# Kernel optimization log

Measured on AMD Instinct MI355X. Metric: run time of the kernel, lower is better.

## Reference

```python
import jax, jax.numpy as jnp
import numpy as np

N_NODES = 200000
N_BONDS = 220000
D = 128


def setup_inputs() -> dict:
    key = jax.random.key(0)
    ks = jax.random.split(key, 8)
    h = jax.random.normal(ks[0], (N_NODES, D), dtype=jnp.float32)
    src = jax.random.randint(ks[1], (N_BONDS,), 0, N_NODES, dtype=jnp.int64)
    dst = jax.random.randint(ks[2], (N_BONDS,), 0, N_NODES, dtype=jnp.int64)
    # MLP params (Sequential: Linear(256,128)+ReLU, Linear(128,128)+ReLU, Linear(128,2))
    W1 = jax.random.normal(ks[3], (2 * D, 128), dtype=jnp.float32) * (1.0 / np.sqrt(2 * D))
    b1 = jnp.zeros((128,), dtype=jnp.float32)
    W2 = jax.random.normal(ks[4], (128, 128), dtype=jnp.float32) * (1.0 / np.sqrt(128))
    b2 = jnp.zeros((128,), dtype=jnp.float32)
    W3 = jax.random.normal(ks[5], (128, 2), dtype=jnp.float32) * (1.0 / np.sqrt(128))
    b3 = jnp.zeros((2,), dtype=jnp.float32)
    return {"h": h, "src": src, "dst": dst,
            "W1": W1, "b1": b1, "W2": W2, "b2": b2, "W3": W3, "b3": b3}


def _mlp(x, W1, b1, W2, b2, W3, b3):
    x = jax.nn.relu(x @ W1 + b1)
    x = jax.nn.relu(x @ W2 + b2)
    return x @ W3 + b3


def reference(h, src, dst, W1, b1, W2, b2, W3, b3):
    # forward edges: (src -> dst); reverse edges: (dst -> src)
    h_src = h[src]            # [E, D] gather
    h_dst = h[dst]            # [E, D] gather
    h_forward = jnp.concatenate([h_src, h_dst], axis=1)  # [E, 2D]
    h_reverse = jnp.concatenate([h_dst, h_src], axis=1)  # [E, 2D]
    return (_mlp(h_forward, W1, b1, W2, b2, W3, b3)
            + _mlp(h_reverse, W1, b1, W2, b2, W3, b3))
```

## Files before the change

### kernel.cpp

```cpp
#include <hip/hip_runtime.h>
#include <hip/hip_bf16.h>
#include <stdint.h>


typedef __attribute__((ext_vector_type(8))) short bf16x8;
typedef __attribute__((ext_vector_type(4))) float f32x4;

__device__ __forceinline__ float bf2f(unsigned u16) {
    union { unsigned u; float f; } v; v.u = u16 << 16;
    return v.f;
}
__device__ __forceinline__ unsigned short f2bf(float f) {
    union { float f; unsigned u; } v; v.f = f;
    unsigned u = v.u;
    unsigned r = u + 0x7FFFu + ((u >> 16) & 1u);
    return (unsigned short)(r >> 16);
}

__device__ __forceinline__ int swz(int f, int c) {
    return f * 128 + ((c ^ (f & 7)) << 3);
}

__device__ __forceinline__ bf16x8 cvt8(const float* p) {
    float4 x = *(const float4*)p;
    float4 y = *(const float4*)(p + 4);
    union { bf16x8 v; __hip_bfloat162 h[4]; } R;
    R.h[0] = __float22bfloat162_rn(float2{x.x, x.y});
    R.h[1] = __float22bfloat162_rn(float2{x.z, x.w});
    R.h[2] = __float22bfloat162_rn(float2{y.x, y.y});
    R.h[3] = __float22bfloat162_rn(float2{y.z, y.w});
    return R.v;
}

__device__ __forceinline__ bf16x8 addrelu8(uint4 a, uint4 b) {
    union { uint4 v; unsigned u[4]; } A, B;
    A.v = a; B.v = b;
    union { bf16x8 v; __hip_bfloat162 h[4]; } R;
#pragma unroll
    for (int i = 0; i < 4; ++i) {
        float a0 = bf2f(A.u[i] & 0xFFFFu), a1 = bf2f(A.u[i] >> 16);
        float b0 = bf2f(B.u[i] & 0xFFFFu), b1 = bf2f(B.u[i] >> 16);
        R.h[i] = __float22bfloat162_rn(float2{fmaxf(a0 + b0, 0.f),
                                              fmaxf(a1 + b1, 0.f)});
    }
    return R.v;
}

#define MFMA(a, b, c) __builtin_amdgcn_mfma_f32_16x16x32_bf16((a), (b), (c), 0, 0, 0)

__global__ void prep_weights(const float* __restrict__ W1,
                             const float* __restrict__ W2,
                             unsigned short* __restrict__ W1t,
                             unsigned short* __restrict__ W2t) {
    int idx = blockIdx.x * 256 + threadIdx.x;
    if (idx < 256 * 128) {
        int j = idx >> 7, k = idx & 127;
        float v = (j < 128) ? W1[k * 128 + j] : W1[(k + 128) * 128 + (j - 128)];
        W1t[idx] = f2bf(v);
    } else {
        int i2 = idx - 256 * 128;
        if (i2 < 128 * 128) {
            int n = i2 >> 7, k = i2 & 127;
            W2t[i2] = f2bf(W2[k * 128 + n]);
        }
    }
}

__global__ __launch_bounds__(512, 2) void node_proj(
    const float* __restrict__ h, const unsigned short* __restrict__ W1t,
    const float* __restrict__ b1, unsigned short* __restrict__ P, int nodes) {
    __shared__ unsigned short W1s[256 * 128];

    int t = threadIdx.x;
    int lane = t & 63;
    int wv = t >> 6;
    int ml = lane & 15, quad = lane >> 4;

    {
        int r = t >> 1, half = t & 1;
        const uint4* src = (const uint4*)(W1t + (size_t)r * 128 + half * 64);
#pragma unroll
        for (int i = 0; i < 8; ++i)
            *(uint4*)(W1s + swz(r, half * 8 + i)) = src[i];
    }

    int node = blockIdx.x * 128 + wv * 16 + ml;
    int nodeL = (node < nodes) ? node : (nodes - 1);
    const float* hrow = h + (size_t)nodeL * 128;
    bf16x8 bfrag[4];
#pragma unroll
    for (int kk = 0; kk < 4; ++kk)
        bfrag[kk] = cvt8(hrow + kk * 32 + quad * 8);

    __syncthreads();

    f32x4 acc[16] = {};
#pragma unroll
    for (int kk = 0; kk < 4; ++kk) {
#pragma unroll
        for (int ct = 0; ct < 16; ++ct) {
            bf16x8 afrag = *(const bf16x8*)(W1s + swz(ct * 16 + ml, kk * 4 + quad));
            acc[ct] = MFMA(afrag, bfrag[kk], acc[ct]);
        }
    }

    if (node < nodes) {
        unsigned short* prow = P + (size_t)node * 256;
#pragma unroll
        for (int ct = 0; ct < 16; ++ct) {
            int fbase = ct * 16 + quad * 4;
            float v0 = acc[ct][0], v1 = acc[ct][1];
            float v2 = acc[ct][2], v3 = acc[ct][3];
            if (fbase >= 128) {
                float4 bv = *(const float4*)(b1 + (fbase - 128));
                v0 += bv.x; v1 += bv.y; v2 += bv.z; v3 += bv.w;
            }
            union { uint2 u; __hip_bfloat162 h2[2]; } o;
            o.h2[0] = __float22bfloat162_rn(float2{v0, v1});
            o.h2[1] = __float22bfloat162_rn(float2{v2, v3});
            *(uint2*)(prow + fbase) = o.u;
        }
    }
}

__global__ __launch_bounds__(512, 2) void edge_mlp(
    const unsigned short* __restrict__ P, const int* __restrict__ src,
    const int* __restrict__ dst, const unsigned short* __restrict__ W2t,
    const float* __restrict__ b2, const float* __restrict__ W3,
    const float* __restrict__ b3, float* __restrict__ out, int E) {
    __shared__ unsigned short W2s[128 * 128];

    int t = threadIdx.x;
    int lane = t & 63;
    int wv = t >> 6;
    int ml = lane & 15, quad = lane >> 4;

    {
        int f = t >> 2, q4 = t & 3;
        const uint4* s = (const uint4*)(W2t + (size_t)f * 128 + q4 * 32);
#pragma unroll
        for (int i = 0; i < 4; ++i)
            *(uint4*)(W2s + swz(f, q4 * 4 + i)) = s[i];
    }

    int e = blockIdx.x * 128 + wv * 16 + ml;
    int ec = (e < E) ? e : (E - 1);
    int si = src[ec], di = dst[ec];
    const unsigned short* Ps = P + (size_t)si * 256;
    const unsigned short* Pd = P + (size_t)di * 256;

    uint4 g[4][4];
#pragma unroll
    for (int kk = 0; kk < 4; ++kk) {
        int ko = kk * 32 + quad * 8;
        g[kk][0] = *(const uint4*)(Ps + ko);
        g[kk][1] = *(const uint4*)(Ps + 128 + ko);
        g[kk][2] = *(const uint4*)(Pd + ko);
        g[kk][3] = *(const uint4*)(Pd + 128 + ko);
    }

    __syncthreads();

    f32x4 acc[2][8] = {};
#pragma unroll
    for (int kk = 0; kk < 4; ++kk) {
        bf16x8 afw = addrelu8(g[kk][0], g[kk][3]);
        bf16x8 arv = addrelu8(g[kk][2], g[kk][1]);
#pragma unroll
        for (int ct = 0; ct < 8; ++ct) {
            bf16x8 bfrag = *(const bf16x8*)(W2s + swz(ct * 16 + ml, kk * 4 + quad));
            acc[0][ct] = MFMA(afw, bfrag, acc[0][ct]);
            acc[1][ct] = MFMA(arv, bfrag, acc[1][ct]);
        }
    }

    float w30[8], w31[8], b2v[8];
#pragma unroll
    for (int ct = 0; ct < 8; ++ct) {
        int c = ct * 16 + ml;
        w30[ct] = W3[c * 2 + 0];
        w31[ct] = W3[c * 2 + 1];
        b2v[ct] = b2[c];
    }
    float p0[2][4], p1[2][4];
#pragma unroll
    for (int rt = 0; rt < 2; ++rt)
#pragma unroll
        for (int reg = 0; reg < 4; ++reg) { p0[rt][reg] = 0.f; p1[rt][reg] = 0.f; }
#pragma unroll
    for (int rt = 0; rt < 2; ++rt)
#pragma unroll
        for (int ct = 0; ct < 8; ++ct)
#pragma unroll
            for (int reg = 0; reg < 4; ++reg) {
                float h2 = fmaxf(acc[rt][ct][reg] + b2v[ct], 0.f);
                p0[rt][reg] += h2 * w30[ct];
                p1[rt][reg] += h2 * w31[ct];
            }
#pragma unroll
    for (int m = 1; m < 16; m <<= 1) {
#pragma unroll
        for (int rt = 0; rt < 2; ++rt)
#pragma unroll
            for (int reg = 0; reg < 4; ++reg) {
                p0[rt][reg] += __shfl_xor(p0[rt][reg], m);
                p1[rt][reg] += __shfl_xor(p1[rt][reg], m);
            }
    }

    if (ml < 2) {
        float bb = 2.f * b3[ml];
#pragma unroll
        for (int reg = 0; reg < 4; ++reg) {
            int ee = blockIdx.x * 128 + wv * 16 + quad * 4 + reg;
            if (ee < E) {
                float v = (ml == 0) ? (p0[0][reg] + p0[1][reg])
                                    : (p1[0][reg] + p1[1][reg]);
                out[(size_t)ee * 2 + ml] = v + bb;
            }
        }
    }
}

extern "C" void kernel_launch(void* const* d_in, const int* in_sizes, int n_in,
                              void* d_out, int out_size, void* d_ws, size_t ws_size,
                              hipStream_t stream) {
    (void)n_in; (void)out_size; (void)ws_size;
    const float* h  = (const float*)d_in[0];
    const int*   sr = (const int*)d_in[1];
    const int*   ds = (const int*)d_in[2];
    const float* W1 = (const float*)d_in[3];
    const float* b1 = (const float*)d_in[4];
    const float* W2 = (const float*)d_in[5];
    const float* b2 = (const float*)d_in[6];
    const float* W3 = (const float*)d_in[7];
    const float* b3 = (const float*)d_in[8];
    float* out = (float*)d_out;

    int nodes = in_sizes[0] / 128;
    int E = in_sizes[1];

    unsigned short* W1t = (unsigned short*)d_ws;
    unsigned short* W2t = W1t + 256 * 128;
    unsigned short* P   = W2t + 128 * 128;

    prep_weights<<<(256 * 128 + 128 * 128 + 255) / 256, 256, 0, stream>>>(W1, W2, W1t, W2t);

    int ntiles = (nodes + 127) / 128;
    node_proj<<<ntiles, 512, 0, stream>>>(h, W1t, b1, P, nodes);

    int etiles = (E + 127) / 128;
    edge_mlp<<<etiles, 512, 0, stream>>>(P, sr, ds, W2t, b2, W3, b3, out, E);
}
```

Measured before the change: 246.2 us.

## Make node and edge kernels persistent with grid-stride tiles and prefetched indices

Result: slower. 602.2 us (+144.6%).

```diff
diff --git a/kernel.cpp b/kernel.cpp
--- a/kernel.cpp
+++ b/kernel.cpp
@@ -66,7 +66,7 @@
     }
 }
 
-__global__ __launch_bounds__(512, 2) void node_proj(
+__global__ __launch_bounds__(512, 4) void node_proj(
     const float* __restrict__ h, const unsigned short* __restrict__ W1t,
     const float* __restrict__ b1, unsigned short* __restrict__ P, int nodes) {
     __shared__ unsigned short W1s[256 * 128];
@@ -78,57 +78,62 @@
 
     {
         int r = t >> 1, half = t & 1;
-        const uint4* src = (const uint4*)(W1t + (size_t)r * 128 + half * 64);
+        const uint4* srcp = (const uint4*)(W1t + (size_t)r * 128 + half * 64);
 #pragma unroll
         for (int i = 0; i < 8; ++i)
-            *(uint4*)(W1s + swz(r, half * 8 + i)) = src[i];
-    }
-
-    int node = blockIdx.x * 128 + wv * 16 + ml;
-    int nodeL = (node < nodes) ? node : (nodes - 1);
-    const float* hrow = h + (size_t)nodeL * 128;
-    bf16x8 bfrag[4];
-#pragma unroll
-    for (int kk = 0; kk < 4; ++kk)
-        bfrag[kk] = cvt8(hrow + kk * 32 + quad * 8);
-
+            *(uint4*)(W1s + swz(r, half * 8 + i)) = srcp[i];
+    }
     __syncthreads();
 
-    f32x4 acc[16] = {};
-#pragma unroll
-    for (int kk = 0; kk < 4; ++kk) {
-#pragma unroll
-        for (int ct = 0; ct < 16; ++ct) {
-            bf16x8 afrag = *(const bf16x8*)(W1s + swz(ct * 16 + ml, kk * 4 + quad));
-            acc[ct] = MFMA(afrag, bfrag[kk], acc[ct]);
-        }
-    }
-
-    if (node < nodes) {
-        unsigned short* prow = P + (size_t)node * 256;
-#pragma unroll
-        for (int ct = 0; ct < 16; ++ct) {
-            int fbase = ct * 16 + quad * 4;
-            float v0 = acc[ct][0], v1 = acc[ct][1];
-            float v2 = acc[ct][2], v3 = acc[ct][3];
-            if (fbase >= 128) {
-                float4 bv = *(const float4*)(b1 + (fbase - 128));
-                v0 += bv.x; v1 += bv.y; v2 += bv.z; v3 += bv.w;
-            }
-            union { uint2 u; __hip_bfloat162 h2[2]; } o;
-            o.h2[0] = __float22bfloat162_rn(float2{v0, v1});
-            o.h2[1] = __float22bfloat162_rn(float2{v2, v3});
-            *(uint2*)(prow + fbase) = o.u;
-        }
-    }
-}
-
-__global__ __launch_bounds__(512, 2) void edge_mlp(
+    int ntiles = (nodes + 127) >> 7;
+    for (int tile = blockIdx.x; tile < ntiles; tile += gridDim.x) {
+        int node = tile * 128 + wv * 16 + ml;
+        int nodeL = (node < nodes) ? node : (nodes - 1);
+        const float* hrow = h + (size_t)nodeL * 128;
+
+        bf16x8 bfrag[4];
+#pragma unroll
+        for (int kk = 0; kk < 4; ++kk)
+            bfrag[kk] = cvt8(hrow + kk * 32 + quad * 8);
+
+        f32x4 acc[16] = {};
+#pragma unroll
+        for (int kk = 0; kk < 4; ++kk) {
+#pragma unroll
+            for (int ct = 0; ct < 16; ++ct) {
+                bf16x8 afrag = *(const bf16x8*)(W1s + swz(ct * 16 + ml, kk * 4 + quad));
+                acc[ct] = MFMA(afrag, bfrag[kk], acc[ct]);
+            }
+        }
+
+        if (node < nodes) {
+            unsigned short* prow = P + (size_t)node * 256;
+#pragma unroll
+            for (int ct = 0; ct < 16; ++ct) {
+                int fbase = ct * 16 + quad * 4;
+                float v0 = acc[ct][0], v1 = acc[ct][1];
+                float v2 = acc[ct][2], v3 = acc[ct][3];
+                if (fbase >= 128) {
+                    float4 bv = *(const float4*)(b1 + (fbase - 128));
+                    v0 += bv.x; v1 += bv.y; v2 += bv.z; v3 += bv.w;
+                }
+                union { uint2 u; __hip_bfloat162 h2[2]; } o;
+                o.h2[0] = __float22bfloat162_rn(float2{v0, v1});
+                o.h2[1] = __float22bfloat162_rn(float2{v2, v3});
+                *(uint2*)(prow + fbase) = o.u;
+            }
+        }
+    }
+}
+
+__global__ __launch_bounds__(512, 4) void edge_mlp(
     const unsigned short* __restrict__ P, const int* __restrict__ src,
     const int* __restrict__ dst, const unsigned short* __restrict__ W2t,
     const float* __restrict__ b2, const float* __restrict__ W3,
     const float* __restrict__ b3, float* __restrict__ out, int E) {
     __shared__ unsigned short W2s[128 * 128];
+    __shared__ float2 cW3[128];
+    __shared__ float  cb2[128];
 
     int t = threadIdx.x;
     int lane = t & 63;
@@ -142,83 +147,90 @@
         for (int i = 0; i < 4; ++i)
             *(uint4*)(W2s + swz(f, q4 * 4 + i)) = s[i];
     }
-
-    int e = blockIdx.x * 128 + wv * 16 + ml;
-    int ec = (e < E) ? e : (E - 1);
-    int si = src[ec], di = dst[ec];
-    const unsigned short* Ps = P + (size_t)si * 256;
-    const unsigned short* Pd = P + (size_t)di * 256;
-
-    uint4 g[4][4];
-#pragma unroll
-    for (int kk = 0; kk < 4; ++kk) {
-        int ko = kk * 32 + quad * 8;
-        g[kk][0] = *(const uint4*)(Ps + ko);
-        g[kk][1] = *(const uint4*)(Ps + 128 + ko);
-        g[kk][2] = *(const uint4*)(Pd + ko);
-        g[kk][3] = *(const uint4*)(Pd + 128 + ko);
-    }
-
+    if (t < 128) {
+        cW3[t] = float2{W3[t * 2 + 0], W3[t * 2 + 1]};
+        cb2[t] = b2[t];
+    }
     __syncthreads();
 
-    f32x4 acc[2][8] = {};
-#pragma unroll
-    for (int kk = 0; kk < 4; ++kk) {
-        bf16x8 afw = addrelu8(g[kk][0], g[kk][3]);
-        bf16x8 arv = addrelu8(g[kk][2], g[kk][1]);
+    int etiles = (E + 127) >> 7;
+
+    int tile = blockIdx.x;
+    int e0 = tile * 128 + wv * 16 + ml;
+    int ec0 = (e0 < E) ? e0 : (E - 1);
+    int si = src[ec0], di = dst[ec0];
+
+    for (; tile < etiles; tile += gridDim.x) {
+        int tn = tile + gridDim.x;
+        int en = tn * 128 + wv * 16 + ml;
+        int ecn = (tn < etiles) ? ((en < E) ? en : (E - 1)) : 0;
+        int sin = src[ecn], din = dst[ecn];
+
+        const unsigned short* Ps = P + (size_t)si * 256;
+        const unsigned short* Pd = P + (size_t)di * 256;
+
+        bf16x8 afw[4], arv[4];
+#pragma unroll
+        for (int kk = 0; kk < 4; ++kk) {
+            int ko = kk * 32 + quad * 8;
+            uint4 slo = *(const uint4*)(Ps + ko);
+            uint4 shi = *(const uint4*)(Ps + 128 + ko);
+            uint4 dlo = *(const uint4*)(Pd + ko);
+            uint4 dhi = *(const uint4*)(Pd + 128 + ko);
+            afw[kk] = addrelu8(slo, dhi);
+            arv[kk] = addrelu8(dlo, shi);
+        }
+
+        f32x4 acc[2][8] = {};
+#pragma unroll
+        for (int kk = 0; kk < 4; ++kk) {
+#pragma unroll
+            for (int ct = 0; ct < 8; ++ct) {
+                bf16x8 bfrag = *(const bf16x8*)(W2s + swz(ct * 16 + ml, kk * 4 + quad));
+                acc[0][ct] = MFMA(afw[kk], bfrag, acc[0][ct]);
+                acc[1][ct] = MFMA(arv[kk], bfrag, acc[1][ct]);
+            }
+        }
+
+        float p0[4] = {0.f, 0.f, 0.f, 0.f};
+        float p1[4] = {0.f, 0.f, 0.f, 0.f};
 #pragma unroll
         for (int ct = 0; ct < 8; ++ct) {
-            bf16x8 bfrag = *(const bf16x8*)(W2s + swz(ct * 16 + ml, kk * 4 + quad));
-            acc[0][ct] = MFMA(afw, bfrag, acc[0][ct]);
-            acc[1][ct] = MFMA(arv, bfrag, acc[1][ct]);
-        }
-    }
-
-    float w30[8], w31[8], b2v[8];
-#pragma unroll
-    for (int ct = 0; ct < 8; ++ct) {
-        int c = ct * 16 + ml;
-        w30[ct] = W3[c * 2 + 0];
-        w31[ct] = W3[c * 2 + 1];
-        b2v[ct] = b2[c];
-    }
-    float p0[2][4], p1[2][4];
-#pragma unroll
-    for (int rt = 0; rt < 2; ++rt)
-#pragma unroll
-        for (int reg = 0; reg < 4; ++reg) { p0[rt][reg] = 0.f; p1[rt][reg] = 0.f; }
-#pragma unroll
-    for (int rt = 0; rt < 2; ++rt)
-#pragma unroll
-        for (int ct = 0; ct < 8; ++ct)
+            int c = ct * 16 + ml;
+            float2 w3 = cW3[c];
+            float bc = cb2[c];
+#pragma unroll
+            for (int rt = 0; rt < 2; ++rt) {
+#pragma unroll
+                for (int reg = 0; reg < 4; ++reg) {
+                    float h2 = fmaxf(acc[rt][ct][reg] + bc, 0.f);
+                    p0[reg] += h2 * w3.x;
+                    p1[reg] += h2 * w3.y;
+                }
+            }
+        }
+#pragma unroll
+        for (int m = 1; m < 16; m <<= 1) {
 #pragma unroll
             for (int reg = 0; reg < 4; ++reg) {
-                float h2 = fmaxf(acc[rt][ct][reg] + b2v[ct], 0.f);
-                p0[rt][reg] += h2 * w30[ct];
-                p1[rt][reg] += h2 * w31[ct];
-            }
-#pragma unroll
-    for (int m = 1; m < 16; m <<= 1) {
-#pragma unroll
-        for (int rt = 0; rt < 2; ++rt)
+                p0[reg] += __shfl_xor(p0[reg], m);
+                p1[reg] += __shfl_xor(p1[reg], m);
+            }
+        }
+
+        if (ml < 2) {
+            float bb = 2.f * b3[ml];
 #pragma unroll
             for (int reg = 0; reg < 4; ++reg) {
-                p0[rt][reg] += __shfl_xor(p0[rt][reg], m);
-                p1[rt][reg] += __shfl_xor(p1[rt][reg], m);
-            }
-    }
-
-    if (ml < 2) {
-        float bb = 2.f * b3[ml];
-#pragma unroll
-        for (int reg = 0; reg < 4; ++reg) {
-            int ee = blockIdx.x * 128 + wv * 16 + quad * 4 + reg;
-            if (ee < E) {
-                float v = (ml == 0) ? (p0[0][reg] + p0[1][reg])
-                                    : (p1[0][reg] + p1[1][reg]);
-                out[(size_t)ee * 2 + ml] = v + bb;
-            }
-        }
+                int ee = tile * 128 + wv * 16 + quad * 4 + reg;
+                if (ee < E) {
+                    float v = (ml == 0) ? p0[reg] : p1[reg];
+                    out[(size_t)ee * 2 + ml] = v + bb;
+                }
+            }
+        }
+
+        si = sin; di = din;
     }
 }
 
@@ -247,8 +259,10 @@
     prep_weights<<<(256 * 128 + 128 * 128 + 255) / 256, 256, 0, stream>>>(W1, W2, W1t, W2t);
 
     int ntiles = (nodes + 127) / 128;
-    node_proj<<<ntiles, 512, 0, stream>>>(h, W1t, b1, P, nodes);
+    int ngrid = ntiles < 512 ? ntiles : 512;
+    node_proj<<<ngrid, 512, 0, stream>>>(h, W1t, b1, P, nodes);
 
     int etiles = (E + 127) / 128;
-    edge_mlp<<<etiles, 512, 0, stream>>>(P, sr, ds, W2t, b2, W3, b3, out, E);
-}
+    int egrid = etiles < 512 ? etiles : 512;
+    edge_mlp<<<egrid, 512, 0, stream>>>(P, sr, ds, W2t, b2, W3, b3, out, E);
+}
```
